# Optimization experiments

Measured on AMD Instinct MI355X. Metric: run time of the kernel, lower is better.

## Reference

```python
import jax, jax.numpy as jnp
import numpy as np

TOTAL = 131072          # total sentences
DIM = 690               # relation_dim (PCNN: 3*230)
NUM_CLASSES = 53        # NYT-10 relations
TOTAL_TYPE = 324        # type_num^2 = 18^2
NUM_BAGS = 8192
ALPHA = 0.9


def setup_inputs() -> dict:
    key = jax.random.key(0)
    ks = jax.random.split(key, 8)
    x = jax.random.normal(ks[0], (TOTAL, DIM), dtype=jnp.float32)
    # strictly increasing bag boundaries: scope[0]=0, scope[-1]=TOTAL, all bags non-empty
    rng = np.random.default_rng(0)
    cuts = np.sort(rng.choice(np.arange(1, TOTAL), NUM_BAGS - 1, replace=False))
    input_scope = jnp.asarray(np.concatenate([[0], cuts, [TOTAL]]), dtype=jnp.int32)
    type_label = jax.random.randint(ks[1], (TOTAL,), 0, TOTAL_TYPE, dtype=jnp.int32)
    query = jax.random.randint(ks[2], (TOTAL,), 0, NUM_CLASSES, dtype=jnp.int32)
    # learned parameters (xavier-ish scale)
    rel_scale = (6.0 / (NUM_CLASSES + DIM)) ** 0.5
    typ_scale = (6.0 / (TOTAL_TYPE + DIM)) ** 0.5
    lin_scale = (6.0 / (DIM + TOTAL_TYPE)) ** 0.5
    relation_weight = jax.random.uniform(ks[3], (NUM_CLASSES, DIM), jnp.float32, -rel_scale, rel_scale)
    type_weight = jax.random.uniform(ks[4], (TOTAL_TYPE, DIM), jnp.float32, -typ_scale, typ_scale)
    bias = jax.random.normal(ks[5], (NUM_CLASSES,), dtype=jnp.float32)
    liner_w = jax.random.uniform(ks[6], (TOTAL_TYPE, DIM), jnp.float32, -lin_scale, lin_scale)
    liner_b = jnp.zeros((TOTAL_TYPE,), dtype=jnp.float32)
    return {
        "x": x, "input_scope": input_scope, "type_label": type_label, "query": query,
        "relation_weight": relation_weight, "type_weight": type_weight, "bias": bias,
        "liner_w": liner_w, "liner_b": liner_b,
    }


def reference(x, input_scope, type_label, query, relation_weight, type_weight, bias, liner_w, liner_b):
    # ---- soft_type (beta != 0 branch) ----
    type_logits = jax.nn.softmax(x @ liner_w.T + liner_b, axis=1)          # [total, T2]
    max_scores = jnp.max(type_logits, axis=1, keepdims=True)               # [total, 1]
    one_hot = jax.nn.one_hot(type_label, TOTAL_TYPE, dtype=type_logits.dtype)
    nscore = type_logits + ALPHA * max_scores * one_hot
    soft_label = jnp.argmax(nscore, axis=1)                                # [total]

    # ---- _train_logits: per-sentence attention logits ----
    xt = x + type_weight[soft_label]                                       # [total, D]
    att = jnp.sum(xt * relation_weight[query], axis=1)                     # [total]

    # ---- bag-wise segment softmax + weighted sum over scopes ----
    seg = jnp.searchsorted(input_scope, jnp.arange(TOTAL), side="right") - 1  # [total] bag ids
    m = jax.ops.segment_max(att, seg, num_segments=NUM_BAGS)               # [bags]
    p = jnp.exp(att - m[seg])
    s = jax.ops.segment_sum(p, seg, num_segments=NUM_BAGS)                 # [bags]
    score = p / s[seg]                                                     # [total]
    bag_repre = jax.ops.segment_sum(score[:, None] * x, seg, num_segments=NUM_BAGS)  # [bags, D]

    # ---- _logits ----
    logits = bag_repre @ relation_weight.T + bias                          # [bags, C]
    return logits, type_logits
```

## Files before the change

kernel.cpp:

```cpp
#include <hip/hip_runtime.h>
#include <hip/hip_bf16.h>

#define TOTAL   131072
#define DIMK    690
#define KPAD    704
#define KSTEPS  22
#define NCLASS  53
#define NTYPE   324
#define NCOLS   377
#define NPAD    384
#define NBAGS   8192
#define ALPHA   0.9f
#define TAU     1e-5f
#define FLAGCAP 32768
#define ZS      388

typedef short  bf16x8 __attribute__((ext_vector_type(8)));
typedef float  f32x4  __attribute__((ext_vector_type(4)));

__device__ __forceinline__ unsigned short bf16_rne(float f) {
    unsigned int u = __float_as_uint(f);
    u = (u + 0x7fffu + ((u >> 16) & 1u)) >> 16;
    return (unsigned short)u;
}
__device__ __forceinline__ float bf16f(unsigned short h) {
    return __uint_as_float(((unsigned int)h) << 16);
}
__device__ __forceinline__ unsigned cvtpk(float a, float b) {
    unsigned r;
    asm("v_cvt_pk_bf16_f32 %0, %1, %2" : "=v"(r) : "v"(a), "v"(b));
    return r;
}

__global__ __launch_bounds__(256) void k_pack(const float* __restrict__ liner_w,
                                              const float* __restrict__ rel_w,
                                              unsigned short* __restrict__ whP,
                                              unsigned short* __restrict__ wlP) {
    const int id = blockIdx.x * 256 + threadIdx.x;
    if (id >= NPAD * KPAD) return;
    const int n = id / KPAD, k = id % KPAD;
    float v = 0.f;
    if (k < DIMK) {
        if (n < NTYPE)      v = liner_w[(size_t)n * DIMK + k];
        else if (n < NCOLS) v = rel_w[(size_t)(n - NTYPE) * DIMK + k];
    }
    const unsigned short hi = bf16_rne(v);
    const unsigned short lo = bf16_rne(v - bf16f(hi));
    const int t = n >> 4, col = n & 15, s = k >> 5, kk = k & 31;
    const int lane = (kk >> 3) * 16 + col, j = kk & 7;
    const int pidx = ((t * KSTEPS + s) * 64 + lane) * 8 + j;
    whP[pidx] = hi;
    wlP[pidx] = lo;
}

__global__ __launch_bounds__(256) void k_table(const float* __restrict__ tw,
                                               const float* __restrict__ rw,
                                               float* __restrict__ table) {
    const int pair = blockIdx.x * 4 + (threadIdx.x >> 6);
    const int lane = threadIdx.x & 63;
    if (pair >= NTYPE * NCLASS) return;
    const int s = pair / NCLASS;
    const int q = pair % NCLASS;
    const float* a = tw + (size_t)s * DIMK;
    const float* b = rw + (size_t)q * DIMK;
    float acc = 0.f;
    for (int k = lane; k < DIMK; k += 64) acc += a[k] * b[k];
#pragma unroll
    for (int off = 32; off; off >>= 1) acc += __shfl_xor(acc, off);
    if (lane == 0) table[pair] = acc;
}

union EpiU {
    unsigned short aS[2][2][2048];
    float          zS[32 * ZS];
};

template<int SC>
__device__ __forceinline__ void epi32(f32x4 (&acc)[4][3],
                                      float* __restrict__ zS,
                                      const float* __restrict__ sB,
                                      const int* __restrict__ type_label,
                                      const int* __restrict__ query,
                                      const float* __restrict__ table,
                                      float* __restrict__ type_logits,
                                      float* __restrict__ att,
                                      float* __restrict__ xr,
                                      int* __restrict__ flagcnt,
                                      int* __restrict__ flaglist,
                                      int base, int wv, int ln) {
    const int q = ln >> 4;

#pragma unroll
    for (int nt = 0; nt < 3; ++nt) {
        const int col = wv * 48 + nt * 16 + (ln & 15);
        const float bb = sB[col];
#pragma unroll
        for (int rg = 0; rg < 4; ++rg) {
            zS[(q * 4 + rg) * ZS + col]      = acc[2 * SC + 0][nt][rg] + bb;
            zS[(16 + q * 4 + rg) * ZS + col] = acc[2 * SC + 1][nt][rg] + bb;
        }
    }
    asm volatile("s_waitcnt lgkmcnt(0)" ::: "memory");
    __builtin_amdgcn_s_barrier();

    for (int rr = 0; rr < 4; ++rr) {
        const int lr   = wv * 4 + rr;
        const int grow = base + SC * 32 + lr;
        const float* zrow = &zS[lr * ZS];

        float z[6];
#pragma unroll
        for (int j = 0; j < 6; ++j) {
            const int c = ln + 64 * j;
            z[j] = (c < NTYPE) ? zrow[c] : -INFINITY;
        }
        float m = -INFINITY;
#pragma unroll
        for (int j = 0; j < 6; ++j) m = fmaxf(m, z[j]);
#pragma unroll
        for (int off = 32; off; off >>= 1) m = fmaxf(m, __shfl_xor(m, off));

        float e[6];
        float ssum = 0.f;
#pragma unroll
        for (int j = 0; j < 6; ++j) {
            const int c = ln + 64 * j;
            e[j] = 0.f;
            if (c < NTYPE) { e[j] = __expf(z[j] - m); ssum += e[j]; }
        }
#pragma unroll
        for (int off = 32; off; off >>= 1) ssum += __shfl_xor(ssum, off);
        const float inv = 1.0f / ssum;

        const int label = type_label[grow];
        float bestv = -INFINITY;
        int   besti = NTYPE;
#pragma unroll
        for (int j = 0; j < 6; ++j) {
            const int c = ln + 64 * j;
            if (c < NTYPE) {
                const float p = e[j] * inv;
                type_logits[(size_t)grow * NTYPE + c] = p;
                const float v = p + ((c == label) ? ALPHA * inv : 0.f);
                if (v > bestv || (v == bestv && c < besti)) { bestv = v; besti = c; }
            }
        }
#pragma unroll
        for (int off = 32; off; off >>= 1) {
            const float ov = __shfl_xor(bestv, off);
            const int   oi = __shfl_xor(besti, off);
            if (ov > bestv || (ov == bestv && oi < besti)) { bestv = ov; besti = oi; }
        }

        float sv = -INFINITY;
#pragma unroll
        for (int j = 0; j < 6; ++j) {
            const int c = ln + 64 * j;
            if (c < NTYPE && c != besti) {
                const float v = e[j] * inv + ((c == label) ? ALPHA * inv : 0.f);
                sv = fmaxf(sv, v);
            }
        }
#pragma unroll
        for (int off = 32; off; off >>= 1) sv = fmaxf(sv, __shfl_xor(sv, off));

        if (ln == 0) {
            const int qq = query[grow];
            att[grow] = zrow[NTYPE + qq] + table[besti * NCLASS + qq];
            if (bestv - sv < TAU) {
                const int ix = atomicAdd(flagcnt, 1);
                if (ix < FLAGCAP) flaglist[ix] = grow;
            }
        }
        if (ln < NCLASS)
            xr[(size_t)grow * NCLASS + ln] = zrow[NTYPE + ln];
    }

    asm volatile("s_waitcnt lgkmcnt(0)" ::: "memory");
    __builtin_amdgcn_s_barrier();
}

__global__ __launch_bounds__(512, 4) void k_main(const float* __restrict__ x,
                                                 const int* __restrict__ type_label,
                                                 const int* __restrict__ query,
                                                 const unsigned short* __restrict__ whP,
                                                 const unsigned short* __restrict__ wlP,
                                                 const float* __restrict__ liner_b,
                                                 const float* __restrict__ table,
                                                 float* __restrict__ type_logits,
                                                 float* __restrict__ att,
                                                 float* __restrict__ xr,
                                                 int* __restrict__ flagcnt,
                                                 int* __restrict__ flaglist) {
    __shared__ __align__(16) EpiU uni;
    __shared__ float sB[NPAD];

    const int tid  = threadIdx.x;
    const int base = blockIdx.x * 64;
    const int wv   = tid >> 6;
    const int ln   = tid & 63;

    const int srow  = tid >> 3;
    const int kpart = tid & 7;

    f32x4 acc[4][3];
#pragma unroll
    for (int mt = 0; mt < 4; ++mt)
#pragma unroll
        for (int nt = 0; nt < 3; ++nt)
            acc[mt][nt] = (f32x4){0.f, 0.f, 0.f, 0.f};

    auto load_x = [&](int s, float (&dst)[4]) {
        const int k0 = s * 32 + kpart * 4;
        const float* xp = x + (size_t)(base + srow) * DIMK + k0;
        if (k0 + 4 <= DIMK) {
            const float2 p0 = *(const float2*)(xp + 0);
            const float2 p1 = *(const float2*)(xp + 2);
            dst[0] = p0.x; dst[1] = p0.y; dst[2] = p1.x; dst[3] = p1.y;
        } else {
#pragma unroll
            for (int j = 0; j < 4; ++j) dst[j] = (k0 + j < DIMK) ? xp[j] : 0.f;
        }
    };
    auto write_a = [&](int nb, const float (&src)[4]) {
        const int kb = kpart >> 1, j0 = (kpart & 1) * 4;
        const int widx = (kb * 64 + srow) * 8 + j0;
        const unsigned h01 = cvtpk(src[0], src[1]);
        const unsigned h23 = cvtpk(src[2], src[3]);
        const float r0 = src[0] - __uint_as_float(h01 << 16);
        const float r1 = src[1] - __uint_as_float(h01 & 0xffff0000u);
        const float r2 = src[2] - __uint_as_float(h23 << 16);
        const float r3 = src[3] - __uint_as_float(h23 & 0xffff0000u);
        const unsigned l01 = cvtpk(r0, r1);
        const unsigned l23 = cvtpk(r2, r3);
        *(uint2*)&uni.aS[nb][0][widx] = make_uint2(h01, h23);
        *(uint2*)&uni.aS[nb][1][widx] = make_uint2(l01, l23);
    };

    float xv[4];
    load_x(0, xv);
    write_a(0, xv);
    for (int c = tid; c < NPAD; c += 512) sB[c] = (c < NTYPE) ? liner_b[c] : 0.f;
    asm volatile("s_waitcnt lgkmcnt(0)" ::: "memory");
    __builtin_amdgcn_s_barrier();

    const int aidx_base = ((ln >> 4) * 64 + (ln & 15)) * 8;
    for (int s = 0; s < KSTEPS; ++s) {
        const int cur = s & 1;
        float xn[4];
        if (s + 1 < KSTEPS) load_x(s + 1, xn);

        bf16x8 ah[4], al[4];
#pragma unroll
        for (int mt = 0; mt < 4; ++mt) {
            const int aidx = aidx_base + mt * 128;
            ah[mt] = *(const bf16x8*)&uni.aS[cur][0][aidx];
            al[mt] = *(const bf16x8*)&uni.aS[cur][1][aidx];
        }
#pragma unroll
        for (int nt = 0; nt < 3; ++nt) {
            const int ntg = wv * 3 + nt;
            const size_t boff = ((size_t)(ntg * KSTEPS + s) * 64 + ln) * 8;
            const bf16x8 bh = *(const bf16x8*)(whP + boff);
            const bf16x8 bl = *(const bf16x8*)(wlP + boff);
#pragma unroll
            for (int mt = 0; mt < 4; ++mt) {
                acc[mt][nt] = __builtin_amdgcn_mfma_f32_16x16x32_bf16(ah[mt], bh, acc[mt][nt], 0, 0, 0);
                acc[mt][nt] = __builtin_amdgcn_mfma_f32_16x16x32_bf16(ah[mt], bl, acc[mt][nt], 0, 0, 0);
                acc[mt][nt] = __builtin_amdgcn_mfma_f32_16x16x32_bf16(al[mt], bh, acc[mt][nt], 0, 0, 0);
            }
        }
        if (s + 1 < KSTEPS) write_a(1 - cur, xn);
        asm volatile("s_waitcnt lgkmcnt(0)" ::: "memory");
        __builtin_amdgcn_s_barrier();
    }

    epi32<0>(acc, uni.zS, sB, type_label, query, table, type_logits, att, xr,
             flagcnt, flaglist, base, wv, ln);
    epi32<1>(acc, uni.zS, sB, type_label, query, table, type_logits, att, xr,
             flagcnt, flaglist, base, wv, ln);
}

__global__ __launch_bounds__(256) void k_fix(const float* __restrict__ x,
                                             const float* __restrict__ liner_w,
                                             const float* __restrict__ liner_b,
                                             const int* __restrict__ type_label,
                                             const int* __restrict__ query,
                                             const float* __restrict__ table,
                                             const float* __restrict__ xr,
                                             const int* __restrict__ flagcnt,
                                             const int* __restrict__ flaglist,
                                             float* __restrict__ att) {
    __shared__ float xs[704];
    __shared__ float zs[NTYPE];
    __shared__ float redm[4];
    __shared__ float redv[4];
    __shared__ int   redi[4];
    const int tid = threadIdx.x;
    const int wv  = tid >> 6;
    const int ln  = tid & 63;
    int count = *flagcnt;
    if (count > FLAGCAP) count = FLAGCAP;

    for (int f = blockIdx.x; f < count; f += gridDim.x) {
        const int row = flaglist[f];
        __syncthreads();
        for (int k = tid; k < 704; k += 256) xs[k] = (k < DIMK) ? x[(size_t)row * DIMK + k] : 0.f;
        __syncthreads();

        for (int ci = 0; ci < 81; ++ci) {
            const int c = wv * 81 + ci;
            const float* w = liner_w + (size_t)c * DIMK;
            float acc = 0.f;
#pragma unroll
            for (int kk = 0; kk < 11; ++kk) {
                const int k = ln + kk * 64;
                const float wval = (k < DIMK) ? w[k] : 0.f;
                acc = fmaf(xs[k], wval, acc);
            }
#pragma unroll
            for (int off = 32; off; off >>= 1) acc += __shfl_xor(acc, off);
            if (ln == 0) zs[c] = acc + liner_b[c];
        }
        __syncthreads();

        float z0 = (tid < NTYPE) ? zs[tid] : -INFINITY;
        const int c1 = tid + 256;
        float z1 = (c1 < NTYPE) ? zs[c1] : -INFINITY;
        float m = fmaxf(z0, z1);
#pragma unroll
        for (int off = 32; off; off >>= 1) m = fmaxf(m, __shfl_xor(m, off));
        if (ln == 0) redm[wv] = m;
        __syncthreads();
        m = fmaxf(fmaxf(redm[0], redm[1]), fmaxf(redm[2], redm[3]));

        const int label = type_label[row];
        const float u0 = (tid < NTYPE) ? (__expf(z0 - m) + ((tid == label) ? ALPHA : 0.f)) : -1.f;
        const float u1 = (c1 < NTYPE)  ? (__expf(z1 - m) + ((c1 == label) ? ALPHA : 0.f))  : -1.f;
        float bv = u0; int bi = tid;
        if (u1 > bv) { bv = u1; bi = c1; }
#pragma unroll
        for (int off = 32; off; off >>= 1) {
            const float ov = __shfl_xor(bv, off);
            const int   oi = __shfl_xor(bi, off);
            if (ov > bv || (ov == bv && oi < bi)) { bv = ov; bi = oi; }
        }
        if (ln == 0) { redv[wv] = bv; redi[wv] = bi; }
        __syncthreads();
        if (tid == 0) {
            float fbv = redv[0]; int fbi = redi[0];
#pragma unroll
            for (int w = 1; w < 4; ++w) {
                if (redv[w] > fbv || (redv[w] == fbv && redi[w] < fbi)) {
                    fbv = redv[w]; fbi = redi[w];
                }
            }
            const int q = query[row];
            att[row] = xr[(size_t)row * NCLASS + q] + table[fbi * NCLASS + q];
        }
    }
}

__global__ __launch_bounds__(64) void k_bag(const float* __restrict__ att,
                                            const float* __restrict__ xr,
                                            const int* __restrict__ scope,
                                            const float* __restrict__ bias,
                                            float* __restrict__ logits) {
    const int b = blockIdx.x;
    const int lane = threadIdx.x;
    const int s0 = scope[b];
    const int s1 = scope[b + 1];

    float m = -INFINITY;
    for (int i = s0 + lane; i < s1; i += 64) m = fmaxf(m, att[i]);
#pragma unroll
    for (int off = 32; off; off >>= 1) m = fmaxf(m, __shfl_xor(m, off));

    float sum = 0.f;
    float acc = 0.f;
    for (int i0 = s0; i0 < s1; i0 += 64) {
        const int n = min(64, s1 - i0);
        float e = 0.f;
        if (lane < n) e = __expf(att[i0 + lane] - m);
        float es = e;
#pragma unroll
        for (int off = 32; off; off >>= 1) es += __shfl_xor(es, off);
        sum += es;
        for (int j = 0; j < n; ++j) {
            const float ej = __shfl(e, j);
            if (lane < NCLASS) acc = fmaf(ej, xr[(size_t)(i0 + j) * NCLASS + lane], acc);
        }
    }
    const float inv = 1.0f / sum;
    if (lane < NCLASS) logits[b * NCLASS + lane] = acc * inv + bias[lane];
}

extern "C" void kernel_launch(void* const* d_in, const int* in_sizes, int n_in,
                              void* d_out, int out_size, void* d_ws, size_t ws_size,
                              hipStream_t stream) {
    const float* x          = (const float*)d_in[0];
    const int*   scope      = (const int*)d_in[1];
    const int*   type_label = (const int*)d_in[2];
    const int*   query      = (const int*)d_in[3];
    const float* rel_w      = (const float*)d_in[4];
    const float* type_w     = (const float*)d_in[5];
    const float* bias       = (const float*)d_in[6];
    const float* liner_w    = (const float*)d_in[7];
    const float* liner_b    = (const float*)d_in[8];

    float* logits      = (float*)d_out;
    float* type_logits = (float*)d_out + NBAGS * NCLASS;

    float* ws = (float*)d_ws;
    float*          table    = ws;
    float*          att      = ws + 17408;
    float*          xr       = ws + 148480;
    unsigned short* whP      = (unsigned short*)(ws + 7095296);
    unsigned short* wlP      = (unsigned short*)(ws + 7230464);
    int*            flagcnt  = (int*)(ws + 7365632);
    int*            flaglist = (int*)(ws + 7365633);

    hipMemsetAsync(flagcnt, 0, sizeof(int), stream);
    hipLaunchKernelGGL(k_pack, dim3((NPAD * KPAD + 255) / 256), dim3(256), 0, stream,
                       liner_w, rel_w, whP, wlP);
    hipLaunchKernelGGL(k_table, dim3((NTYPE * NCLASS + 3) / 4), dim3(256), 0, stream,
                       type_w, rel_w, table);
    hipLaunchKernelGGL(k_main, dim3(TOTAL / 64), dim3(512), 0, stream,
                       x, type_label, query, whP, wlP, liner_b, table,
                       type_logits, att, xr, flagcnt, flaglist);
    hipLaunchKernelGGL(k_fix, dim3(1024), dim3(256), 0, stream,
                       x, liner_w, liner_b, type_label, query, table, xr,
                       flagcnt, flaglist, att);
    hipLaunchKernelGGL(k_bag, dim3(NBAGS), dim3(64), 0, stream,
                       att, xr, scope, bias, logits);
}
```

Before: 443.3 us.

## Load A fragments directly from global per wave, dropping LDS staging and barriers

Each wave now reads its x rows straight from global memory into MFMA A-fragment registers and does the bf16 hi/lo split there. This removes the shared-memory double buffer and the per-k-step barriers. The eight waves each reload and convert the same 64 rows, so global/L2 traffic and conversion work grow about eightfold. Launch bounds drop from 4 to 3 blocks per SM, and the bias is now read from global memory.

```diff
diff --git a/kernel.cpp b/kernel.cpp
--- a/kernel.cpp
+++ b/kernel.cpp
@@ -70,15 +70,10 @@
     if (lane == 0) table[pair] = acc;
 }
 
-union EpiU {
-    unsigned short aS[2][2][2048];
-    float          zS[32 * ZS];
-};
-
 template<int SC>
 __device__ __forceinline__ void epi32(f32x4 (&acc)[4][3],
                                       float* __restrict__ zS,
-                                      const float* __restrict__ sB,
+                                      const float* __restrict__ liner_b,
                                       const int* __restrict__ type_label,
                                       const int* __restrict__ query,
                                       const float* __restrict__ table,
@@ -93,7 +88,7 @@
 #pragma unroll
     for (int nt = 0; nt < 3; ++nt) {
         const int col = wv * 48 + nt * 16 + (ln & 15);
-        const float bb = sB[col];
+        const float bb = (col < NTYPE) ? liner_b[col] : 0.f;
 #pragma unroll
         for (int rg = 0; rg < 4; ++rg) {
             zS[(q * 4 + rg) * ZS + col]      = acc[2 * SC + 0][nt][rg] + bb;
@@ -180,7 +175,7 @@
     __builtin_amdgcn_s_barrier();
 }
 
-__global__ __launch_bounds__(512, 4) void k_main(const float* __restrict__ x,
+__global__ __launch_bounds__(512, 3) void k_main(const float* __restrict__ x,
                                                  const int* __restrict__ type_label,
                                                  const int* __restrict__ query,
                                                  const unsigned short* __restrict__ whP,
@@ -192,17 +187,13 @@
                                                  float* __restrict__ xr,
                                                  int* __restrict__ flagcnt,
                                                  int* __restrict__ flaglist) {
-    __shared__ __align__(16) EpiU uni;
-    __shared__ float sB[NPAD];
+    __shared__ __align__(16) float zS[32 * ZS];
 
     const int tid  = threadIdx.x;
     const int base = blockIdx.x * 64;
     const int wv   = tid >> 6;
     const int ln   = tid & 63;
 
-    const int srow  = tid >> 3;
-    const int kpart = tid & 7;
-
     f32x4 acc[4][3];
 #pragma unroll
     for (int mt = 0; mt < 4; ++mt)
@@ -210,59 +201,58 @@
         for (int nt = 0; nt < 3; ++nt)
             acc[mt][nt] = (f32x4){0.f, 0.f, 0.f, 0.f};
 
-    auto load_x = [&](int s, float (&dst)[4]) {
-        const int k0 = s * 32 + kpart * 4;
-        const float* xp = x + (size_t)(base + srow) * DIMK + k0;
-        if (k0 + 4 <= DIMK) {
-            const float2 p0 = *(const float2*)(xp + 0);
-            const float2 p1 = *(const float2*)(xp + 2);
-            dst[0] = p0.x; dst[1] = p0.y; dst[2] = p1.x; dst[3] = p1.y;
-        } else {
-#pragma unroll
-            for (int j = 0; j < 4; ++j) dst[j] = (k0 + j < DIMK) ? xp[j] : 0.f;
-        }
-    };
-    auto write_a = [&](int nb, const float (&src)[4]) {
-        const int kb = kpart >> 1, j0 = (kpart & 1) * 4;
-        const int widx = (kb * 64 + srow) * 8 + j0;
-        const unsigned h01 = cvtpk(src[0], src[1]);
-        const unsigned h23 = cvtpk(src[2], src[3]);
-        const float r0 = src[0] - __uint_as_float(h01 << 16);
-        const float r1 = src[1] - __uint_as_float(h01 & 0xffff0000u);
-        const float r2 = src[2] - __uint_as_float(h23 << 16);
-        const float r3 = src[3] - __uint_as_float(h23 & 0xffff0000u);
-        const unsigned l01 = cvtpk(r0, r1);
-        const unsigned l23 = cvtpk(r2, r3);
-        *(uint2*)&uni.aS[nb][0][widx] = make_uint2(h01, h23);
-        *(uint2*)&uni.aS[nb][1][widx] = make_uint2(l01, l23);
-    };
-
-    float xv[4];
-    load_x(0, xv);
-    write_a(0, xv);
-    for (int c = tid; c < NPAD; c += 512) sB[c] = (c < NTYPE) ? liner_b[c] : 0.f;
-    asm volatile("s_waitcnt lgkmcnt(0)" ::: "memory");
-    __builtin_amdgcn_s_barrier();
-
-    const int aidx_base = ((ln >> 4) * 64 + (ln & 15)) * 8;
+    const unsigned short* whB[3];
+    const unsigned short* wlB[3];
+#pragma unroll
+    for (int nt = 0; nt < 3; ++nt) {
+        const int ntg = wv * 3 + nt;
+        whB[nt] = whP + ((size_t)(ntg * KSTEPS) * 64 + ln) * 8;
+        wlB[nt] = wlP + ((size_t)(ntg * KSTEPS) * 64 + ln) * 8;
+    }
+
+    const int arow = ln & 15;
+    const int kgrp = (ln >> 4) * 8;
+    const float* xrow0 = x + (size_t)(base + arow) * DIMK;
+
     for (int s = 0; s < KSTEPS; ++s) {
-        const int cur = s & 1;
-        float xn[4];
-        if (s + 1 < KSTEPS) load_x(s + 1, xn);
+        const int k0 = s * 32 + kgrp;
 
         bf16x8 ah[4], al[4];
 #pragma unroll
         for (int mt = 0; mt < 4; ++mt) {
-            const int aidx = aidx_base + mt * 128;
-            ah[mt] = *(const bf16x8*)&uni.aS[cur][0][aidx];
-            al[mt] = *(const bf16x8*)&uni.aS[cur][1][aidx];
-        }
+            const float* xp = xrow0 + (size_t)(mt * 16) * DIMK + k0;
+            float f[8];
+            if (k0 + 8 <= DIMK) {
+                const float2 p0 = *(const float2*)(xp + 0);
+                const float2 p1 = *(const float2*)(xp + 2);
+                const float2 p2 = *(const float2*)(xp + 4);
+                const float2 p3 = *(const float2*)(xp + 6);
+                f[0] = p0.x; f[1] = p0.y; f[2] = p1.x; f[3] = p1.y;
+                f[4] = p2.x; f[5] = p2.y; f[6] = p3.x; f[7] = p3.y;
+            } else {
+#pragma unroll
+                for (int j = 0; j < 8; ++j) f[j] = (k0 + j < DIMK) ? xp[j] : 0.f;
+            }
+            unsigned h[4], l[4];
+#pragma unroll
+            for (int i = 0; i < 4; ++i) {
+                h[i] = cvtpk(f[2 * i], f[2 * i + 1]);
+                const float r0 = f[2 * i]     - __uint_as_float(h[i] << 16);
+                const float r1 = f[2 * i + 1] - __uint_as_float(h[i] & 0xffff0000u);
+                l[i] = cvtpk(r0, r1);
+            }
+            union { uint4 u; bf16x8 v; } ch, cl;
+            ch.u = make_uint4(h[0], h[1], h[2], h[3]);
+            cl.u = make_uint4(l[0], l[1], l[2], l[3]);
+            ah[mt] = ch.v;
+            al[mt] = cl.v;
+        }
+
+        const int so = s * 512;
 #pragma unroll
         for (int nt = 0; nt < 3; ++nt) {
-            const int ntg = wv * 3 + nt;
-            const size_t boff = ((size_t)(ntg * KSTEPS + s) * 64 + ln) * 8;
-            const bf16x8 bh = *(const bf16x8*)(whP + boff);
-            const bf16x8 bl = *(const bf16x8*)(wlP + boff);
+            const bf16x8 bh = *(const bf16x8*)(whB[nt] + so);
+            const bf16x8 bl = *(const bf16x8*)(wlB[nt] + so);
 #pragma unroll
             for (int mt = 0; mt < 4; ++mt) {
                 acc[mt][nt] = __builtin_amdgcn_mfma_f32_16x16x32_bf16(ah[mt], bh, acc[mt][nt], 0, 0, 0);
@@ -270,14 +260,11 @@
                 acc[mt][nt] = __builtin_amdgcn_mfma_f32_16x16x32_bf16(al[mt], bh, acc[mt][nt], 0, 0, 0);
             }
         }
-        if (s + 1 < KSTEPS) write_a(1 - cur, xn);
-        asm volatile("s_waitcnt lgkmcnt(0)" ::: "memory");
-        __builtin_amdgcn_s_barrier();
-    }
-
-    epi32<0>(acc, uni.zS, sB, type_label, query, table, type_logits, att, xr,
+    }
+
+    epi32<0>(acc, zS, liner_b, type_label, query, table, type_logits, att, xr,
              flagcnt, flaglist, base, wv, ln);
-    epi32<1>(acc, uni.zS, sB, type_label, query, table, type_logits, att, xr,
+    epi32<1>(acc, zS, liner_b, type_label, query, table, type_logits, att, xr,
              flagcnt, flaglist, base, wv, ln);
 }
 
```

New measurement: 552.6 us. 1.25x slower.
